# Kernel optimization log

Hardware: AMD Instinct MI355X
Metric: run time of the kernel (lower is better)

Reference implementation:

```python
import jax, jax.numpy as jnp
import numpy as np

B, S, D, H = 4, 2048, 1024, 16
DH = D // H


def setup_inputs() -> dict:
    key = jax.random.key(0)
    ks = jax.random.split(key, 10)
    init = lambda k, shape: jax.random.normal(k, shape, dtype=jnp.float32) * 0.02
    return {
        "x": jax.random.normal(ks[0], (B, S, D), dtype=jnp.float32),
        "attention_mask": jnp.ones((B, S), dtype=bool),
        "use_causal_mask": 1,
        "Wq": init(ks[1], (D, D)), "bq": jnp.zeros((D,), jnp.float32),
        "Wk": init(ks[2], (D, D)), "bk": jnp.zeros((D,), jnp.float32),
        "Wv": init(ks[3], (D, D)), "bv": jnp.zeros((D,), jnp.float32),
        "Wo": init(ks[4], (D, D)), "bo": jnp.zeros((D,), jnp.float32),
    }


def _split_heads(t):
    # (B, S, D) -> (B, H, S, DH)
    b, s, d = t.shape
    return t.reshape(b, s, H, DH).transpose(0, 2, 1, 3)


def reference(x, attention_mask, use_causal_mask, Wq, bq, Wk, bk, Wv, bv, Wo, bo):
    q = _split_heads(x @ Wq + bq)  # (B, H, S, DH)
    k = _split_heads(x @ Wk + bk)
    v = _split_heads(x @ Wv + bv)

    scale = 1.0 / jnp.sqrt(jnp.asarray(DH, dtype=x.dtype))
    scores = jnp.einsum("bhqd,bhkd->bhqk", q, k) * scale  # (B, H, S, S)

    blocked = jnp.finfo(scores.dtype).min
    if use_causal_mask:
        causal = jnp.tril(jnp.ones((S, S), dtype=bool))[None, None]
        scores = jnp.where(causal, scores, blocked)
    # attention_mask: (B, S) over keys
    scores = jnp.where(attention_mask[:, None, None, :], scores, blocked)

    weights = jax.nn.softmax(scores, axis=-1)
    attn = jnp.einsum("bhqk,bhkd->bhqd", weights, v)  # (B, H, S, DH)
    attn = attn.transpose(0, 2, 1, 3).reshape(B, S, D)  # combine heads
    return attn @ Wo + bo
```

## Files before the change

### kernel.cpp

```cpp
#include <hip/hip_runtime.h>
#include <hip/hip_bf16.h>
#include <cstdint>
#include <cstddef>


#define BB 4
#define SS 2048
#define DD 1024
#define HH 16
#define DHH 64

typedef float f32x4 __attribute__((ext_vector_type(4)));
typedef __bf16 bf16x8 __attribute__((ext_vector_type(8)));

#define QSCALE 0.1803368801111204f

__device__ __forceinline__ unsigned short f2bf(float f) {
  union { __hip_bfloat16 h; unsigned short u; } cv;
  cv.h = __float2bfloat16(f);
  return cv.u;
}

__device__ __forceinline__ float fexp2(float x) { return __builtin_amdgcn_exp2f(x); }

__device__ __forceinline__ void gload_lds16(const void* g, void* l) {
  __builtin_amdgcn_global_load_lds((const __attribute__((address_space(1))) void*)g,
                                   (__attribute__((address_space(3))) void*)l,
                                   16, 0, 0);
}

__device__ __forceinline__ void wait_vm4() { asm volatile("s_waitcnt vmcnt(4)" ::: "memory"); }
__device__ __forceinline__ void wait_vm8() { asm volatile("s_waitcnt vmcnt(8)" ::: "memory"); }
__device__ __forceinline__ void wait_vm0() { asm volatile("s_waitcnt vmcnt(0)" ::: "memory"); }
__device__ __forceinline__ void block_barrier() {
  asm volatile("" ::: "memory");
  __builtin_amdgcn_s_barrier();
  asm volatile("" ::: "memory");
}

__global__ void k_f32_to_bf16(const float* __restrict__ in,
                              unsigned short* __restrict__ out, int n8) {
  int i = blockIdx.x * blockDim.x + threadIdx.x;
  if (i >= n8) return;
  const float4* p = (const float4*)in + (size_t)i * 2;
  float4 a = p[0], b = p[1];
  union { unsigned short u[8]; uint4 v; } r;
  r.u[0] = f2bf(a.x); r.u[1] = f2bf(a.y); r.u[2] = f2bf(a.z); r.u[3] = f2bf(a.w);
  r.u[4] = f2bf(b.x); r.u[5] = f2bf(b.y); r.u[6] = f2bf(b.z); r.u[7] = f2bf(b.w);
  ((uint4*)out)[i] = r.v;
}

__global__ void k_transpose_w4(const float* __restrict__ Wq, const float* __restrict__ Wk,
                               const float* __restrict__ Wv, const float* __restrict__ Wo,
                               unsigned short* __restrict__ Wqkvt,
                               unsigned short* __restrict__ Wot) {
  __shared__ float t[64][65];
  const int z = blockIdx.z;
  const float* W = (z == 0) ? Wq : (z == 1) ? Wk : (z == 2) ? Wv : Wo;
  unsigned short* dst = (z < 3) ? (Wqkvt + (size_t)z * DD * DD) : Wot;
  int bx = blockIdx.x * 64;
  int by = blockIdx.y * 64;
  int c  = threadIdx.x & 63;
  int r0 = threadIdx.x >> 6;
#pragma unroll
  for (int r = r0; r < 64; r += 4)
    t[r][c] = W[(size_t)(by + r) * DD + bx + c];
  __syncthreads();
#pragma unroll
  for (int r = r0; r < 64; r += 4)
    dst[(size_t)(bx + r) * DD + by + c] = f2bf(t[c][r]);
}

template <int MODE, int GN>
__global__ __launch_bounds__(256) void k_gemm(const unsigned short* __restrict__ A,
                                              const unsigned short* __restrict__ Bt,
                                              const float* __restrict__ b0,
                                              const float* __restrict__ b1,
                                              const float* __restrict__ b2,
                                              void* __restrict__ out0,
                                              void* __restrict__ out1,
                                              void* __restrict__ out2) {
  constexpr int Kd = 1024;
  constexpr int NSTEP = Kd / 64;
  __shared__ unsigned short As[2][128 * 64];
  __shared__ unsigned short Bs[2][128 * 64];
  const int tid = threadIdx.x;
  const int wave = tid >> 6, lane = tid & 63;
  const int hw = blockIdx.x;
  const int xcd = hw & 7;
  const int j = hw >> 3;
  const int super = j >> 6;
  const int rem = j & 63;
  const int bm = (xcd * 8 + (rem >> 3)) * 128;
  const int bn = (super * 8 + (rem & 7)) * 128;
  const int wm = (wave >> 1) * 64, wn = (wave & 1) * 64;

  f32x4 acc[4][4] = {};

  const int srow = wave * 8 + (lane >> 3);
  const int csw = lane & 7;

  auto stage = [&](int buf, int k0) {
#pragma unroll
    for (int q = 0; q < 4; q++) {
      int r = q * 32 + srow;
      int clog = csw ^ (r & 7);
      gload_lds16(A + (size_t)(bm + r) * Kd + k0 + clog * 8, &As[buf][q * 2048 + wave * 512]);
      gload_lds16(Bt + (size_t)(bn + r) * Kd + k0 + clog * 8, &Bs[buf][q * 2048 + wave * 512]);
    }
  };

  stage(0, 0);
  for (int ks = 0; ks < NSTEP; ks++) {
    if (ks + 1 < NSTEP) {
      stage((ks + 1) & 1, (ks + 1) * 64);
      wait_vm8();
    } else {
      wait_vm0();
    }
    block_barrier();
    const unsigned short* Asb = As[ks & 1];
    const unsigned short* Bsb = Bs[ks & 1];
#pragma unroll
    for (int kk = 0; kk < 2; kk++) {
      bf16x8 af[4], bfr[4];
      int ch = (kk << 2) | (lane >> 4);
#pragma unroll
      for (int i = 0; i < 4; i++) {
        int row = wm + i * 16 + (lane & 15);
        af[i] = *(const bf16x8*)&Asb[row * 64 + ((ch ^ (row & 7)) << 3)];
      }
#pragma unroll
      for (int j2 = 0; j2 < 4; j2++) {
        int col = wn + j2 * 16 + (lane & 15);
        bfr[j2] = *(const bf16x8*)&Bsb[col * 64 + ((ch ^ (col & 7)) << 3)];
      }
#pragma unroll
      for (int i = 0; i < 4; i++)
#pragma unroll
        for (int j2 = 0; j2 < 4; j2++)
          acc[i][j2] = __builtin_amdgcn_mfma_f32_16x16x32_bf16(af[i], bfr[j2], acc[i][j2], 0, 0, 0);
    }
    block_barrier();
  }

  const int mat = bn >> 10;
  const float* bias = (MODE == 2) ? b0 : (mat == 0 ? b0 : (mat == 1 ? b1 : b2));
  const float scale = (MODE == 0 && mat == 0) ? QSCALE : 1.0f;
#pragma unroll
  for (int i = 0; i < 4; i++) {
#pragma unroll
    for (int j2 = 0; j2 < 4; j2++) {
      int col = bn + wn + j2 * 16 + (lane & 15);
      int c2 = col & 1023;
      float bv = bias[MODE == 2 ? col : c2];
      int row0 = bm + wm + i * 16 + ((lane >> 4) << 2);
      if (MODE == 0 && mat == 2) {
        int b = row0 >> 11, s0 = row0 & 2047, h = c2 >> 6, dh = c2 & 63;
        ushort4 pk;
        pk.x = f2bf(acc[i][j2][0] + bv);
        pk.y = f2bf(acc[i][j2][1] + bv);
        pk.z = f2bf(acc[i][j2][2] + bv);
        pk.w = f2bf(acc[i][j2][3] + bv);
        *(ushort4*)((unsigned short*)out2 + (((size_t)(b * HH + h) * DHH + dh) << 11) + s0) = pk;
      } else {
#pragma unroll
        for (int reg = 0; reg < 4; reg++) {
          int row = row0 + reg;
          float v = (acc[i][j2][reg] + bv) * scale;
          if (MODE == 0) {
            int b = row >> 11, s = row & 2047, h = c2 >> 6, dh = c2 & 63;
            unsigned short* dst = (unsigned short*)(mat == 0 ? out0 : out1);
            dst[(((size_t)(b * HH + h) * SS + s) << 6) + dh] = f2bf(v);
          } else {
            ((float*)out0)[(size_t)row * DD + col] = v;
          }
        }
      }
    }
  }
}

__global__ __launch_bounds__(256) void k_attn(const unsigned short* __restrict__ Q,
                                              const unsigned short* __restrict__ Kb,
                                              const unsigned short* __restrict__ Vt,
                                              unsigned short* __restrict__ O,
                                              const int* __restrict__ use_causal) {
  __shared__ unsigned short Ks[2][64 * 64];
  __shared__ unsigned short Vs[2][64 * 64];
  __shared__ unsigned short Ps[4 * 16 * 64];
  const int hw = blockIdx.x;
  const int bh = (hw & 7) | ((hw >> 7) << 3);
  const int pr = (hw >> 3) & 15;
  const int b = bh >> 4, h = bh & 15;
  const int tid = threadIdx.x, wave = tid >> 6, lane = tid & 63;
  const int lanelo = lane & 15, lanehi = lane >> 4;
  const bool causal = (use_causal[0] != 0);

  const unsigned short* Kg = Kb + (size_t)bh * SS * DHH;
  const unsigned short* Vg = Vt + (size_t)bh * DHH * SS;
  const int srow = wave * 8 + (lane >> 3);
  const int csw = lane & 7;
  const int qlocal = wave * 16 + lanelo;

  auto stage = [&](int buf, int kt) {
#pragma unroll
    for (int q = 0; q < 2; q++) {
      int r = q * 32 + srow;
      int clog = csw ^ (r & 7);
      gload_lds16(Kg + (size_t)(kt * 64 + r) * DHH + clog * 8, &Ks[buf][q * 2048 + wave * 512]);
      gload_lds16(Vg + (size_t)r * SS + kt * 64 + clog * 8, &Vs[buf][q * 2048 + wave * 512]);
    }
  };

  for (int pass = 0; pass < 2; pass++) {
    const int qt = pass ? (SS / 64 - 1 - pr) : pr;
    const unsigned short* Qg = Q + ((size_t)bh * SS + qt * 64) * DHH;

    bf16x8 qf0, qf1;
    {
      const unsigned short* qrow = Qg + (wave * 16 + lanelo) * DHH + (lanehi << 3);
      qf0 = *(const bf16x8*)qrow;
      qf1 = *(const bf16x8*)(qrow + 32);
    }

    float m = -1e30f, ls = 0.f;
    f32x4 o[4] = {};
    const int ntile = causal ? (qt + 1) : (SS / 64);

    stage(0, 0);
    for (int kt = 0; kt < ntile; kt++) {
      if (kt + 1 < ntile) {
        stage((kt + 1) & 1, kt + 1);
        wait_vm4();
      } else {
        wait_vm0();
      }
      block_barrier();
      const unsigned short* Ksb = Ks[kt & 1];
      const unsigned short* Vsb = Vs[kt & 1];

      f32x4 scT[4];
#pragma unroll
      for (int kb = 0; kb < 4; kb++) {
        int key = kb * 16 + lanelo;
        bf16x8 a0 = *(const bf16x8*)&Ksb[key * 64 + ((lanehi ^ (key & 7)) << 3)];
        bf16x8 a1 = *(const bf16x8*)&Ksb[key * 64 + (((lanehi + 4) ^ (key & 7)) << 3)];
        f32x4 t = {};
        t = __builtin_amdgcn_mfma_f32_16x16x32_bf16(a0, qf0, t, 0, 0, 0);
        t = __builtin_amdgcn_mfma_f32_16x16x32_bf16(a1, qf1, t, 0, 0, 0);
        scT[kb] = t;
      }

      const bool needmask = causal && (kt == qt);
      float mx = -3.0e38f;
#pragma unroll
      for (int kb = 0; kb < 4; kb++)
#pragma unroll
        for (int reg = 0; reg < 4; reg++) {
          float v = scT[kb][reg];
          if (needmask && (kb * 16 + 4 * lanehi + reg) > qlocal) v = -3.0e38f;
          scT[kb][reg] = v;
          mx = fmaxf(mx, v);
        }

      if (__any((int)(mx > m + 8.0f))) {
        float rmx = fmaxf(mx, __shfl_xor(mx, 16, 64));
        rmx = fmaxf(rmx, __shfl_xor(rmx, 32, 64));
        float mnew = fmaxf(m, rmx);
        float al = fexp2(m - mnew);
        m = mnew;
        ls *= al;
        float alr[4];
#pragma unroll
        for (int reg = 0; reg < 4; reg++)
          alr[reg] = __shfl(al, (lanehi << 2) + reg, 64);
#pragma unroll
        for (int dhb = 0; dhb < 4; dhb++) {
          f32x4 t = o[dhb];
          t[0] *= alr[0]; t[1] *= alr[1]; t[2] *= alr[2]; t[3] *= alr[3];
          o[dhb] = t;
        }
      }

      unsigned short* Pw = &Ps[wave * 1024];
#pragma unroll
      for (int kb = 0; kb < 4; kb++) {
        ushort4 pk;
        float p0 = fexp2(scT[kb][0] - m);
        float p1 = fexp2(scT[kb][1] - m);
        float p2 = fexp2(scT[kb][2] - m);
        float p3 = fexp2(scT[kb][3] - m);
        ls += (p0 + p1) + (p2 + p3);
        pk.x = f2bf(p0); pk.y = f2bf(p1); pk.z = f2bf(p2); pk.w = f2bf(p3);
        int chunk = (kb * 2 + (lanehi >> 1)) ^ (lanelo & 7);
        *(ushort4*)&Pw[lanelo * 64 + (chunk << 3) + ((lanehi & 1) << 2)] = pk;
      }

      int ar = lanelo;
      bf16x8 pa0 = *(const bf16x8*)&Pw[ar * 64 + ((lanehi ^ (ar & 7)) << 3)];
      bf16x8 pa1 = *(const bf16x8*)&Pw[ar * 64 + (((lanehi + 4) ^ (ar & 7)) << 3)];
#pragma unroll
      for (int dhb = 0; dhb < 4; dhb++) {
        int dh = dhb * 16 + lanelo;
        bf16x8 v0 = *(const bf16x8*)&Vsb[dh * 64 + ((lanehi ^ (dh & 7)) << 3)];
        bf16x8 v1 = *(const bf16x8*)&Vsb[dh * 64 + (((lanehi + 4) ^ (dh & 7)) << 3)];
        o[dhb] = __builtin_amdgcn_mfma_f32_16x16x32_bf16(pa0, v0, o[dhb], 0, 0, 0);
        o[dhb] = __builtin_amdgcn_mfma_f32_16x16x32_bf16(pa1, v1, o[dhb], 0, 0, 0);
      }
      block_barrier();
    }

    float t = ls + __shfl_xor(ls, 16, 64);
    t += __shfl_xor(t, 32, 64);
    float inv = 1.0f / t;
    float invr[4];
#pragma unroll
    for (int reg = 0; reg < 4; reg++)
      invr[reg] = __shfl(inv, (lanehi << 2) + reg, 64);
#pragma unroll
    for (int dhb = 0; dhb < 4; dhb++)
#pragma unroll
      for (int reg = 0; reg < 4; reg++) {
        int s = qt * 64 + wave * 16 + (lanehi << 2) + reg;
        int dh = dhb * 16 + lanelo;
        O[((size_t)(b * SS + s)) * DD + h * DHH + dh] = f2bf(o[dhb][reg] * invr[reg]);
      }
  }
}

extern "C" void kernel_launch(void* const* d_in, const int* in_sizes, int n_in,
                              void* d_out, int out_size, void* d_ws, size_t ws_size,
                              hipStream_t stream) {
  const float* x = (const float*)d_in[0];
  const int* use_causal = (const int*)d_in[2];
  const float* Wq = (const float*)d_in[3];
  const float* bq = (const float*)d_in[4];
  const float* Wk = (const float*)d_in[5];
  const float* bk = (const float*)d_in[6];
  const float* Wv = (const float*)d_in[7];
  const float* bv = (const float*)d_in[8];
  const float* Wo = (const float*)d_in[9];
  const float* bo = (const float*)d_in[10];

  char* ws = (char*)d_ws;
  unsigned short* xb    = (unsigned short*)(ws);
  unsigned short* Wqkvt = (unsigned short*)(ws + (16ull << 20));
  unsigned short* Wot   = (unsigned short*)(ws + (22ull << 20));
  unsigned short* Qb    = (unsigned short*)(ws + (24ull << 20));
  unsigned short* Kbuf  = (unsigned short*)(ws + (40ull << 20));
  unsigned short* Vtb   = (unsigned short*)(ws + (56ull << 20));
  unsigned short* Attn  = (unsigned short*)(ws + (72ull << 20));

  int n8 = BB * SS * DD / 8;
  k_f32_to_bf16<<<(n8 + 255) / 256, 256, 0, stream>>>(x, xb, n8);

  k_transpose_w4<<<dim3(16, 16, 4), 256, 0, stream>>>(Wq, Wk, Wv, Wo, Wqkvt, Wot);

  k_gemm<0, 24><<<dim3(64 * 24), 256, 0, stream>>>(xb, Wqkvt, bq, bk, bv, Qb, Kbuf, Vtb);

  k_attn<<<dim3(1024), 256, 0, stream>>>(Qb, Kbuf, Vtb, Attn, use_causal);

  k_gemm<2, 8><<<dim3(64 * 8), 256, 0, stream>>>(Attn, Wot, bo, nullptr, nullptr, d_out, nullptr, nullptr);
}
```

Before: 173.6 us.

## Use two waves per attention block, each computing 32 query rows

Measured after the change: 175.3 us. No clear change (+1.0%).

```diff
diff --git a/kernel.cpp b/kernel.cpp
--- a/kernel.cpp
+++ b/kernel.cpp
@@ -181,7 +181,7 @@
   }
 }
 
-__global__ __launch_bounds__(256) void k_attn(const unsigned short* __restrict__ Q,
+__global__ __launch_bounds__(128) void k_attn(const unsigned short* __restrict__ Q,
                                               const unsigned short* __restrict__ Kb,
                                               const unsigned short* __restrict__ Vt,
                                               unsigned short* __restrict__ O,
@@ -199,40 +199,40 @@
 
   const unsigned short* Kg = Kb + (size_t)bh * SS * DHH;
   const unsigned short* Vg = Vt + (size_t)bh * DHH * SS;
-  const int srow = wave * 8 + (lane >> 3);
+  const int srow8 = wave * 8 + (lane >> 3);
   const int csw = lane & 7;
-  const int qlocal = wave * 16 + lanelo;
 
   auto stage = [&](int buf, int kt) {
 #pragma unroll
-    for (int q = 0; q < 2; q++) {
-      int r = q * 32 + srow;
+    for (int q = 0; q < 4; q++) {
+      int r = q * 16 + srow8;
       int clog = csw ^ (r & 7);
-      gload_lds16(Kg + (size_t)(kt * 64 + r) * DHH + clog * 8, &Ks[buf][q * 2048 + wave * 512]);
-      gload_lds16(Vg + (size_t)r * SS + kt * 64 + clog * 8, &Vs[buf][q * 2048 + wave * 512]);
+      gload_lds16(Kg + (size_t)(kt * 64 + r) * DHH + clog * 8, &Ks[buf][q * 1024 + wave * 512]);
+      gload_lds16(Vg + (size_t)r * SS + kt * 64 + clog * 8, &Vs[buf][q * 1024 + wave * 512]);
     }
   };
 
   for (int pass = 0; pass < 2; pass++) {
-    const int qt = pass ? (SS / 64 - 1 - pr) : pr;
+    const int qt = pass ? (31 - pr) : pr;
     const unsigned short* Qg = Q + ((size_t)bh * SS + qt * 64) * DHH;
 
-    bf16x8 qf0, qf1;
-    {
-      const unsigned short* qrow = Qg + (wave * 16 + lanelo) * DHH + (lanehi << 3);
-      qf0 = *(const bf16x8*)qrow;
-      qf1 = *(const bf16x8*)(qrow + 32);
-    }
-
-    float m = -1e30f, ls = 0.f;
-    f32x4 o[4] = {};
-    const int ntile = causal ? (qt + 1) : (SS / 64);
+    bf16x8 qf[2][2];
+#pragma unroll
+    for (int qb = 0; qb < 2; qb++) {
+      const unsigned short* qrow = Qg + (wave * 32 + qb * 16 + lanelo) * DHH + (lanehi << 3);
+      qf[qb][0] = *(const bf16x8*)qrow;
+      qf[qb][1] = *(const bf16x8*)(qrow + 32);
+    }
+
+    float m[2] = {-1e30f, -1e30f}, ls[2] = {0.f, 0.f};
+    f32x4 o[2][4] = {};
+    const int ntile = causal ? (qt + 1) : 32;
 
     stage(0, 0);
     for (int kt = 0; kt < ntile; kt++) {
       if (kt + 1 < ntile) {
         stage((kt + 1) & 1, kt + 1);
-        wait_vm4();
+        wait_vm8();
       } else {
         wait_vm0();
       }
@@ -240,92 +240,122 @@
       const unsigned short* Ksb = Ks[kt & 1];
       const unsigned short* Vsb = Vs[kt & 1];
 
-      f32x4 scT[4];
+      f32x4 scT[2][4];
+      __builtin_amdgcn_s_setprio(1);
 #pragma unroll
       for (int kb = 0; kb < 4; kb++) {
         int key = kb * 16 + lanelo;
         bf16x8 a0 = *(const bf16x8*)&Ksb[key * 64 + ((lanehi ^ (key & 7)) << 3)];
         bf16x8 a1 = *(const bf16x8*)&Ksb[key * 64 + (((lanehi + 4) ^ (key & 7)) << 3)];
-        f32x4 t = {};
-        t = __builtin_amdgcn_mfma_f32_16x16x32_bf16(a0, qf0, t, 0, 0, 0);
-        t = __builtin_amdgcn_mfma_f32_16x16x32_bf16(a1, qf1, t, 0, 0, 0);
-        scT[kb] = t;
-      }
+        f32x4 t0 = {}, t1 = {};
+        t0 = __builtin_amdgcn_mfma_f32_16x16x32_bf16(a0, qf[0][0], t0, 0, 0, 0);
+        t0 = __builtin_amdgcn_mfma_f32_16x16x32_bf16(a1, qf[0][1], t0, 0, 0, 0);
+        t1 = __builtin_amdgcn_mfma_f32_16x16x32_bf16(a0, qf[1][0], t1, 0, 0, 0);
+        t1 = __builtin_amdgcn_mfma_f32_16x16x32_bf16(a1, qf[1][1], t1, 0, 0, 0);
+        scT[0][kb] = t0;
+        scT[1][kb] = t1;
+      }
+      __builtin_amdgcn_s_setprio(0);
 
       const bool needmask = causal && (kt == qt);
-      float mx = -3.0e38f;
-#pragma unroll
-      for (int kb = 0; kb < 4; kb++)
-#pragma unroll
-        for (int reg = 0; reg < 4; reg++) {
-          float v = scT[kb][reg];
-          if (needmask && (kb * 16 + 4 * lanehi + reg) > qlocal) v = -3.0e38f;
-          scT[kb][reg] = v;
-          mx = fmaxf(mx, v);
+      float mx[2];
+      bool need = false;
+#pragma unroll
+      for (int qb = 0; qb < 2; qb++) {
+        int qlocal = wave * 32 + qb * 16 + lanelo;
+        float x = -3.0e38f;
+#pragma unroll
+        for (int kb = 0; kb < 4; kb++)
+#pragma unroll
+          for (int reg = 0; reg < 4; reg++) {
+            float v = scT[qb][kb][reg];
+            if (needmask && (kb * 16 + 4 * lanehi + reg) > qlocal) v = -3.0e38f;
+            scT[qb][kb][reg] = v;
+            x = fmaxf(x, v);
+          }
+        mx[qb] = x;
+        need = need || (x > m[qb] + 8.0f);
+      }
+
+      if (__any((int)need)) {
+#pragma unroll
+        for (int qb = 0; qb < 2; qb++) {
+          float rmx = fmaxf(mx[qb], __shfl_xor(mx[qb], 16, 64));
+          rmx = fmaxf(rmx, __shfl_xor(rmx, 32, 64));
+          float mnew = fmaxf(m[qb], rmx);
+          float al = fexp2(m[qb] - mnew);
+          m[qb] = mnew;
+          ls[qb] *= al;
+          float alr[4];
+#pragma unroll
+          for (int reg = 0; reg < 4; reg++)
+            alr[reg] = __shfl(al, (lanehi << 2) + reg, 64);
+#pragma unroll
+          for (int dhb = 0; dhb < 4; dhb++) {
+            f32x4 t = o[qb][dhb];
+            t[0] *= alr[0]; t[1] *= alr[1]; t[2] *= alr[2]; t[3] *= alr[3];
+            o[qb][dhb] = t;
+          }
         }
-
-      if (__any((int)(mx > m + 8.0f))) {
-        float rmx = fmaxf(mx, __shfl_xor(mx, 16, 64));
-        rmx = fmaxf(rmx, __shfl_xor(rmx, 32, 64));
-        float mnew = fmaxf(m, rmx);
-        float al = fexp2(m - mnew);
-        m = mnew;
-        ls *= al;
-        float alr[4];
-#pragma unroll
-        for (int reg = 0; reg < 4; reg++)
-          alr[reg] = __shfl(al, (lanehi << 2) + reg, 64);
-#pragma unroll
-        for (int dhb = 0; dhb < 4; dhb++) {
-          f32x4 t = o[dhb];
-          t[0] *= alr[0]; t[1] *= alr[1]; t[2] *= alr[2]; t[3] *= alr[3];
-          o[dhb] = t;
+      }
+
+#pragma unroll
+      for (int qb = 0; qb < 2; qb++) {
+        unsigned short* Pw = &Ps[(wave * 2 + qb) * 1024];
+#pragma unroll
+        for (int kb = 0; kb < 4; kb++) {
+          float p0 = fexp2(scT[qb][kb][0] - m[qb]);
+          float p1 = fexp2(scT[qb][kb][1] - m[qb]);
+          float p2 = fexp2(scT[qb][kb][2] - m[qb]);
+          float p3 = fexp2(scT[qb][kb][3] - m[qb]);
+          ls[qb] += (p0 + p1) + (p2 + p3);
+          ushort4 pk;
+          pk.x = f2bf(p0); pk.y = f2bf(p1); pk.z = f2bf(p2); pk.w = f2bf(p3);
+          int chunk = (kb * 2 + (lanehi >> 1)) ^ (lanelo & 7);
+          *(ushort4*)&Pw[lanelo * 64 + (chunk << 3) + ((lanehi & 1) << 2)] = pk;
         }
       }
 
-      unsigned short* Pw = &Ps[wave * 1024];
-#pragma unroll
-      for (int kb = 0; kb < 4; kb++) {
-        ushort4 pk;
-        float p0 = fexp2(scT[kb][0] - m);
-        float p1 = fexp2(scT[kb][1] - m);
-        float p2 = fexp2(scT[kb][2] - m);
-        float p3 = fexp2(scT[kb][3] - m);
-        ls += (p0 + p1) + (p2 + p3);
-        pk.x = f2bf(p0); pk.y = f2bf(p1); pk.z = f2bf(p2); pk.w = f2bf(p3);
-        int chunk = (kb * 2 + (lanehi >> 1)) ^ (lanelo & 7);
-        *(ushort4*)&Pw[lanelo * 64 + (chunk << 3) + ((lanehi & 1) << 2)] = pk;
-      }
-
-      int ar = lanelo;
-      bf16x8 pa0 = *(const bf16x8*)&Pw[ar * 64 + ((lanehi ^ (ar & 7)) << 3)];
-      bf16x8 pa1 = *(const bf16x8*)&Pw[ar * 64 + (((lanehi + 4) ^ (ar & 7)) << 3)];
+      bf16x8 pa[2][2];
+#pragma unroll
+      for (int qb = 0; qb < 2; qb++) {
+        const unsigned short* Pw = &Ps[(wave * 2 + qb) * 1024];
+        pa[qb][0] = *(const bf16x8*)&Pw[lanelo * 64 + ((lanehi ^ (lanelo & 7)) << 3)];
+        pa[qb][1] = *(const bf16x8*)&Pw[lanelo * 64 + (((lanehi + 4) ^ (lanelo & 7)) << 3)];
+      }
+      __builtin_amdgcn_s_setprio(1);
 #pragma unroll
       for (int dhb = 0; dhb < 4; dhb++) {
         int dh = dhb * 16 + lanelo;
         bf16x8 v0 = *(const bf16x8*)&Vsb[dh * 64 + ((lanehi ^ (dh & 7)) << 3)];
         bf16x8 v1 = *(const bf16x8*)&Vsb[dh * 64 + (((lanehi + 4) ^ (dh & 7)) << 3)];
-        o[dhb] = __builtin_amdgcn_mfma_f32_16x16x32_bf16(pa0, v0, o[dhb], 0, 0, 0);
-        o[dhb] = __builtin_amdgcn_mfma_f32_16x16x32_bf16(pa1, v1, o[dhb], 0, 0, 0);
-      }
+        o[0][dhb] = __builtin_amdgcn_mfma_f32_16x16x32_bf16(pa[0][0], v0, o[0][dhb], 0, 0, 0);
+        o[0][dhb] = __builtin_amdgcn_mfma_f32_16x16x32_bf16(pa[0][1], v1, o[0][dhb], 0, 0, 0);
+        o[1][dhb] = __builtin_amdgcn_mfma_f32_16x16x32_bf16(pa[1][0], v0, o[1][dhb], 0, 0, 0);
+        o[1][dhb] = __builtin_amdgcn_mfma_f32_16x16x32_bf16(pa[1][1], v1, o[1][dhb], 0, 0, 0);
+      }
+      __builtin_amdgcn_s_setprio(0);
       block_barrier();
     }
 
-    float t = ls + __shfl_xor(ls, 16, 64);
-    t += __shfl_xor(t, 32, 64);
-    float inv = 1.0f / t;
-    float invr[4];
-#pragma unroll
-    for (int reg = 0; reg < 4; reg++)
-      invr[reg] = __shfl(inv, (lanehi << 2) + reg, 64);
-#pragma unroll
-    for (int dhb = 0; dhb < 4; dhb++)
-#pragma unroll
-      for (int reg = 0; reg < 4; reg++) {
-        int s = qt * 64 + wave * 16 + (lanehi << 2) + reg;
-        int dh = dhb * 16 + lanelo;
-        O[((size_t)(b * SS + s)) * DD + h * DHH + dh] = f2bf(o[dhb][reg] * invr[reg]);
-      }
+#pragma unroll
+    for (int qb = 0; qb < 2; qb++) {
+      float t = ls[qb] + __shfl_xor(ls[qb], 16, 64);
+      t += __shfl_xor(t, 32, 64);
+      float inv = 1.0f / t;
+      float invr[4];
+#pragma unroll
+      for (int reg = 0; reg < 4; reg++)
+        invr[reg] = __shfl(inv, (lanehi << 2) + reg, 64);
+#pragma unroll
+      for (int dhb = 0; dhb < 4; dhb++)
+#pragma unroll
+        for (int reg = 0; reg < 4; reg++) {
+          int s = qt * 64 + wave * 32 + qb * 16 + (lanehi << 2) + reg;
+          int dh = dhb * 16 + lanelo;
+          O[((size_t)(b * SS + s)) * DD + h * DHH + dh] = f2bf(o[qb][dhb][reg] * invr[reg]);
+        }
+    }
   }
 }
 
@@ -359,7 +389,7 @@
 
   k_gemm<0, 24><<<dim3(64 * 24), 256, 0, stream>>>(xb, Wqkvt, bq, bk, bv, Qb, Kbuf, Vtb);
 
-  k_attn<<<dim3(1024), 256, 0, stream>>>(Qb, Kbuf, Vtb, Attn, use_causal);
+  k_attn<<<dim3(1024), 128, 0, stream>>>(Qb, Kbuf, Vtb, Attn, use_causal);
 
   k_gemm<2, 8><<<dim3(64 * 8), 256, 0, stream>>>(Attn, Wot, bo, nullptr, nullptr, d_out, nullptr, nullptr);
 }
```

## Fuse paired causal query tiles into one pass sharing K/V tile loads

Applied to the files above, without the earlier changes.

Result: slower. 195.1 us (+12.4%).

```diff
diff --git a/kernel.cpp b/kernel.cpp
--- a/kernel.cpp
+++ b/kernel.cpp
@@ -203,6 +203,10 @@
   const int csw = lane & 7;
   const int qlocal = wave * 16 + lanelo;
 
+  const int qt0 = pr, qt1 = 31 - pr;
+  const int kA = causal ? qt0 : 31;
+  const int kend = causal ? qt1 : 31;
+
   auto stage = [&](int buf, int kt) {
 #pragma unroll
     for (int q = 0; q < 2; q++) {
@@ -213,105 +217,167 @@
     }
   };
 
-  for (int pass = 0; pass < 2; pass++) {
-    const int qt = pass ? (SS / 64 - 1 - pr) : pr;
-    const unsigned short* Qg = Q + ((size_t)bh * SS + qt * 64) * DHH;
-
-    bf16x8 qf0, qf1;
-    {
-      const unsigned short* qrow = Qg + (wave * 16 + lanelo) * DHH + (lanehi << 3);
-      qf0 = *(const bf16x8*)qrow;
-      qf1 = *(const bf16x8*)(qrow + 32);
-    }
-
-    float m = -1e30f, ls = 0.f;
-    f32x4 o[4] = {};
-    const int ntile = causal ? (qt + 1) : (SS / 64);
-
-    stage(0, 0);
-    for (int kt = 0; kt < ntile; kt++) {
-      if (kt + 1 < ntile) {
-        stage((kt + 1) & 1, kt + 1);
-        wait_vm4();
-      } else {
-        wait_vm0();
-      }
-      block_barrier();
-      const unsigned short* Ksb = Ks[kt & 1];
-      const unsigned short* Vsb = Vs[kt & 1];
-
-      f32x4 scT[4];
-#pragma unroll
-      for (int kb = 0; kb < 4; kb++) {
-        int key = kb * 16 + lanelo;
-        bf16x8 a0 = *(const bf16x8*)&Ksb[key * 64 + ((lanehi ^ (key & 7)) << 3)];
-        bf16x8 a1 = *(const bf16x8*)&Ksb[key * 64 + (((lanehi + 4) ^ (key & 7)) << 3)];
-        f32x4 t = {};
-        t = __builtin_amdgcn_mfma_f32_16x16x32_bf16(a0, qf0, t, 0, 0, 0);
-        t = __builtin_amdgcn_mfma_f32_16x16x32_bf16(a1, qf1, t, 0, 0, 0);
-        scT[kb] = t;
-      }
-
-      const bool needmask = causal && (kt == qt);
+  bf16x8 qfA0, qfA1, qfB0, qfB1;
+  {
+    const unsigned short* qa = Q + ((size_t)bh * SS + qt0 * 64 + wave * 16 + lanelo) * DHH + (lanehi << 3);
+    qfA0 = *(const bf16x8*)qa;
+    qfA1 = *(const bf16x8*)(qa + 32);
+    const unsigned short* qb = Q + ((size_t)bh * SS + qt1 * 64 + wave * 16 + lanelo) * DHH + (lanehi << 3);
+    qfB0 = *(const bf16x8*)qb;
+    qfB1 = *(const bf16x8*)(qb + 32);
+  }
+
+  float mA = -1e30f, lsA = 0.f, mB = -1e30f, lsB = 0.f;
+  f32x4 oA[4] = {}, oB[4] = {};
+
+  stage(0, 0);
+  for (int kt = 0; kt <= kend; kt++) {
+    if (kt < kend) {
+      stage((kt + 1) & 1, kt + 1);
+      wait_vm4();
+    } else {
+      wait_vm0();
+    }
+    block_barrier();
+    const unsigned short* Ksb = Ks[kt & 1];
+    const unsigned short* Vsb = Vs[kt & 1];
+    const bool doA = (kt <= kA);
+
+    f32x4 sA[4], sB[4];
+    __builtin_amdgcn_s_setprio(1);
+#pragma unroll
+    for (int kb = 0; kb < 4; kb++) {
+      int key = kb * 16 + lanelo;
+      bf16x8 a0 = *(const bf16x8*)&Ksb[key * 64 + ((lanehi ^ (key & 7)) << 3)];
+      bf16x8 a1 = *(const bf16x8*)&Ksb[key * 64 + (((lanehi + 4) ^ (key & 7)) << 3)];
+      f32x4 t = {};
+      t = __builtin_amdgcn_mfma_f32_16x16x32_bf16(a0, qfB0, t, 0, 0, 0);
+      t = __builtin_amdgcn_mfma_f32_16x16x32_bf16(a1, qfB1, t, 0, 0, 0);
+      sB[kb] = t;
+      if (doA) {
+        f32x4 u = {};
+        u = __builtin_amdgcn_mfma_f32_16x16x32_bf16(a0, qfA0, u, 0, 0, 0);
+        u = __builtin_amdgcn_mfma_f32_16x16x32_bf16(a1, qfA1, u, 0, 0, 0);
+        sA[kb] = u;
+      }
+    }
+    __builtin_amdgcn_s_setprio(0);
+
+    unsigned short* Pw = &Ps[wave * 1024];
+    bf16x8 paA0, paA1, paB0, paB1;
+
+    if (doA) {
+      const bool needmask = causal && (kt == qt0);
       float mx = -3.0e38f;
 #pragma unroll
       for (int kb = 0; kb < 4; kb++)
 #pragma unroll
         for (int reg = 0; reg < 4; reg++) {
-          float v = scT[kb][reg];
+          float v = sA[kb][reg];
           if (needmask && (kb * 16 + 4 * lanehi + reg) > qlocal) v = -3.0e38f;
-          scT[kb][reg] = v;
+          sA[kb][reg] = v;
           mx = fmaxf(mx, v);
         }
-
-      if (__any((int)(mx > m + 8.0f))) {
+      if (__any((int)(mx > mA + 8.0f))) {
         float rmx = fmaxf(mx, __shfl_xor(mx, 16, 64));
         rmx = fmaxf(rmx, __shfl_xor(rmx, 32, 64));
-        float mnew = fmaxf(m, rmx);
-        float al = fexp2(m - mnew);
-        m = mnew;
-        ls *= al;
+        float mnew = fmaxf(mA, rmx);
+        float al = fexp2(mA - mnew);
+        mA = mnew;
+        lsA *= al;
         float alr[4];
 #pragma unroll
         for (int reg = 0; reg < 4; reg++)
           alr[reg] = __shfl(al, (lanehi << 2) + reg, 64);
 #pragma unroll
         for (int dhb = 0; dhb < 4; dhb++) {
-          f32x4 t = o[dhb];
+          f32x4 t = oA[dhb];
           t[0] *= alr[0]; t[1] *= alr[1]; t[2] *= alr[2]; t[3] *= alr[3];
-          o[dhb] = t;
+          oA[dhb] = t;
         }
       }
-
-      unsigned short* Pw = &Ps[wave * 1024];
 #pragma unroll
       for (int kb = 0; kb < 4; kb++) {
+        float p0 = fexp2(sA[kb][0] - mA);
+        float p1 = fexp2(sA[kb][1] - mA);
+        float p2 = fexp2(sA[kb][2] - mA);
+        float p3 = fexp2(sA[kb][3] - mA);
+        lsA += (p0 + p1) + (p2 + p3);
         ushort4 pk;
-        float p0 = fexp2(scT[kb][0] - m);
-        float p1 = fexp2(scT[kb][1] - m);
-        float p2 = fexp2(scT[kb][2] - m);
-        float p3 = fexp2(scT[kb][3] - m);
-        ls += (p0 + p1) + (p2 + p3);
         pk.x = f2bf(p0); pk.y = f2bf(p1); pk.z = f2bf(p2); pk.w = f2bf(p3);
         int chunk = (kb * 2 + (lanehi >> 1)) ^ (lanelo & 7);
         *(ushort4*)&Pw[lanelo * 64 + (chunk << 3) + ((lanehi & 1) << 2)] = pk;
       }
-
-      int ar = lanelo;
-      bf16x8 pa0 = *(const bf16x8*)&Pw[ar * 64 + ((lanehi ^ (ar & 7)) << 3)];
-      bf16x8 pa1 = *(const bf16x8*)&Pw[ar * 64 + (((lanehi + 4) ^ (ar & 7)) << 3)];
-#pragma unroll
-      for (int dhb = 0; dhb < 4; dhb++) {
-        int dh = dhb * 16 + lanelo;
-        bf16x8 v0 = *(const bf16x8*)&Vsb[dh * 64 + ((lanehi ^ (dh & 7)) << 3)];
-        bf16x8 v1 = *(const bf16x8*)&Vsb[dh * 64 + (((lanehi + 4) ^ (dh & 7)) << 3)];
-        o[dhb] = __builtin_amdgcn_mfma_f32_16x16x32_bf16(pa0, v0, o[dhb], 0, 0, 0);
-        o[dhb] = __builtin_amdgcn_mfma_f32_16x16x32_bf16(pa1, v1, o[dhb], 0, 0, 0);
-      }
-      block_barrier();
-    }
-
-    float t = ls + __shfl_xor(ls, 16, 64);
+      paA0 = *(const bf16x8*)&Pw[lanelo * 64 + ((lanehi ^ (lanelo & 7)) << 3)];
+      paA1 = *(const bf16x8*)&Pw[lanelo * 64 + (((lanehi + 4) ^ (lanelo & 7)) << 3)];
+    }
+
+    {
+      const bool needmask = causal && (kt == qt1);
+      float mx = -3.0e38f;
+#pragma unroll
+      for (int kb = 0; kb < 4; kb++)
+#pragma unroll
+        for (int reg = 0; reg < 4; reg++) {
+          float v = sB[kb][reg];
+          if (needmask && (kb * 16 + 4 * lanehi + reg) > qlocal) v = -3.0e38f;
+          sB[kb][reg] = v;
+          mx = fmaxf(mx, v);
+        }
+      if (__any((int)(mx > mB + 8.0f))) {
+        float rmx = fmaxf(mx, __shfl_xor(mx, 16, 64));
+        rmx = fmaxf(rmx, __shfl_xor(rmx, 32, 64));
+        float mnew = fmaxf(mB, rmx);
+        float al = fexp2(mB - mnew);
+        mB = mnew;
+        lsB *= al;
+        float alr[4];
+#pragma unroll
+        for (int reg = 0; reg < 4; reg++)
+          alr[reg] = __shfl(al, (lanehi << 2) + reg, 64);
+#pragma unroll
+        for (int dhb = 0; dhb < 4; dhb++) {
+          f32x4 t = oB[dhb];
+          t[0] *= alr[0]; t[1] *= alr[1]; t[2] *= alr[2]; t[3] *= alr[3];
+          oB[dhb] = t;
+        }
+      }
+      asm volatile("" ::: "memory");
+#pragma unroll
+      for (int kb = 0; kb < 4; kb++) {
+        float p0 = fexp2(sB[kb][0] - mB);
+        float p1 = fexp2(sB[kb][1] - mB);
+        float p2 = fexp2(sB[kb][2] - mB);
+        float p3 = fexp2(sB[kb][3] - mB);
+        lsB += (p0 + p1) + (p2 + p3);
+        ushort4 pk;
+        pk.x = f2bf(p0); pk.y = f2bf(p1); pk.z = f2bf(p2); pk.w = f2bf(p3);
+        int chunk = (kb * 2 + (lanehi >> 1)) ^ (lanelo & 7);
+        *(ushort4*)&Pw[lanelo * 64 + (chunk << 3) + ((lanehi & 1) << 2)] = pk;
+      }
+      paB0 = *(const bf16x8*)&Pw[lanelo * 64 + ((lanehi ^ (lanelo & 7)) << 3)];
+      paB1 = *(const bf16x8*)&Pw[lanelo * 64 + (((lanehi + 4) ^ (lanelo & 7)) << 3)];
+    }
+
+    __builtin_amdgcn_s_setprio(1);
+#pragma unroll
+    for (int dhb = 0; dhb < 4; dhb++) {
+      int dh = dhb * 16 + lanelo;
+      bf16x8 v0 = *(const bf16x8*)&Vsb[dh * 64 + ((lanehi ^ (dh & 7)) << 3)];
+      bf16x8 v1 = *(const bf16x8*)&Vsb[dh * 64 + (((lanehi + 4) ^ (dh & 7)) << 3)];
+      oB[dhb] = __builtin_amdgcn_mfma_f32_16x16x32_bf16(paB0, v0, oB[dhb], 0, 0, 0);
+      oB[dhb] = __builtin_amdgcn_mfma_f32_16x16x32_bf16(paB1, v1, oB[dhb], 0, 0, 0);
+      if (doA) {
+        oA[dhb] = __builtin_amdgcn_mfma_f32_16x16x32_bf16(paA0, v0, oA[dhb], 0, 0, 0);
+        oA[dhb] = __builtin_amdgcn_mfma_f32_16x16x32_bf16(paA1, v1, oA[dhb], 0, 0, 0);
+      }
+    }
+    __builtin_amdgcn_s_setprio(0);
+    block_barrier();
+  }
+
+  {
+    float t = lsA + __shfl_xor(lsA, 16, 64);
     t += __shfl_xor(t, 32, 64);
     float inv = 1.0f / t;
     float invr[4];
@@ -322,9 +388,26 @@
     for (int dhb = 0; dhb < 4; dhb++)
 #pragma unroll
       for (int reg = 0; reg < 4; reg++) {
-        int s = qt * 64 + wave * 16 + (lanehi << 2) + reg;
+        int s = qt0 * 64 + wave * 16 + (lanehi << 2) + reg;
         int dh = dhb * 16 + lanelo;
-        O[((size_t)(b * SS + s)) * DD + h * DHH + dh] = f2bf(o[dhb][reg] * invr[reg]);
+        O[((size_t)(b * SS + s)) * DD + h * DHH + dh] = f2bf(oA[dhb][reg] * invr[reg]);
+      }
+  }
+  {
+    float t = lsB + __shfl_xor(lsB, 16, 64);
+    t += __shfl_xor(t, 32, 64);
+    float inv = 1.0f / t;
+    float invr[4];
+#pragma unroll
+    for (int reg = 0; reg < 4; reg++)
+      invr[reg] = __shfl(inv, (lanehi << 2) + reg, 64);
+#pragma unroll
+    for (int dhb = 0; dhb < 4; dhb++)
+#pragma unroll
+      for (int reg = 0; reg < 4; reg++) {
+        int s = qt1 * 64 + wave * 16 + (lanehi << 2) + reg;
+        int dh = dhb * 16 + lanelo;
+        O[((size_t)(b * SS + s)) * DD + h * DHH + dh] = f2bf(oB[dhb][reg] * invr[reg]);
       }
   }
 }
```

## Compute softmax row sums via MFMA with ones vector and add setprio hints

Applied to the files above, without the earlier changes.

Result: no change. 172.6 us (-0.6%).

```diff
diff --git a/kernel.cpp b/kernel.cpp
--- a/kernel.cpp
+++ b/kernel.cpp
@@ -203,6 +203,10 @@
   const int csw = lane & 7;
   const int qlocal = wave * 16 + lanelo;
 
+  bf16x8 vones;
+#pragma unroll
+  for (int i = 0; i < 8; i++) vones[i] = (__bf16)1.0f;
+
   auto stage = [&](int buf, int kt) {
 #pragma unroll
     for (int q = 0; q < 2; q++) {
@@ -224,8 +228,9 @@
       qf1 = *(const bf16x8*)(qrow + 32);
     }
 
-    float m = -1e30f, ls = 0.f;
+    float m = -1e30f;
     f32x4 o[4] = {};
+    f32x4 o_ls = {};
     const int ntile = causal ? (qt + 1) : (SS / 64);
 
     stage(0, 0);
@@ -241,6 +246,7 @@
       const unsigned short* Vsb = Vs[kt & 1];
 
       f32x4 scT[4];
+      __builtin_amdgcn_s_setprio(1);
 #pragma unroll
       for (int kb = 0; kb < 4; kb++) {
         int key = kb * 16 + lanelo;
@@ -251,18 +257,28 @@
         t = __builtin_amdgcn_mfma_f32_16x16x32_bf16(a1, qf1, t, 0, 0, 0);
         scT[kb] = t;
       }
-
-      const bool needmask = causal && (kt == qt);
-      float mx = -3.0e38f;
-#pragma unroll
-      for (int kb = 0; kb < 4; kb++)
-#pragma unroll
-        for (int reg = 0; reg < 4; reg++) {
-          float v = scT[kb][reg];
-          if (needmask && (kb * 16 + 4 * lanehi + reg) > qlocal) v = -3.0e38f;
-          scT[kb][reg] = v;
-          mx = fmaxf(mx, v);
-        }
+      __builtin_amdgcn_s_setprio(0);
+
+      float mx;
+      if (causal && (kt == qt)) {
+        mx = -3.0e38f;
+#pragma unroll
+        for (int kb = 0; kb < 4; kb++)
+#pragma unroll
+          for (int reg = 0; reg < 4; reg++) {
+            float v = scT[kb][reg];
+            if ((kb * 16 + 4 * lanehi + reg) > qlocal) v = -3.0e38f;
+            scT[kb][reg] = v;
+            mx = fmaxf(mx, v);
+          }
+      } else {
+        float t0 = fmaxf(fmaxf(scT[0][0], scT[0][1]), scT[0][2]);
+        float t1 = fmaxf(fmaxf(scT[0][3], scT[1][0]), scT[1][1]);
+        float t2 = fmaxf(fmaxf(scT[1][2], scT[1][3]), scT[2][0]);
+        float t3 = fmaxf(fmaxf(scT[2][1], scT[2][2]), scT[2][3]);
+        float t4 = fmaxf(fmaxf(scT[3][0], scT[3][1]), scT[3][2]);
+        mx = fmaxf(fmaxf(fmaxf(t0, t1), t2), fmaxf(fmaxf(t3, t4), scT[3][3]));
+      }
 
       if (__any((int)(mx > m + 8.0f))) {
         float rmx = fmaxf(mx, __shfl_xor(mx, 16, 64));
@@ -270,7 +286,6 @@
         float mnew = fmaxf(m, rmx);
         float al = fexp2(m - mnew);
         m = mnew;
-        ls *= al;
         float alr[4];
 #pragma unroll
         for (int reg = 0; reg < 4; reg++)
@@ -281,18 +296,17 @@
           t[0] *= alr[0]; t[1] *= alr[1]; t[2] *= alr[2]; t[3] *= alr[3];
           o[dhb] = t;
         }
+        o_ls[0] *= alr[0]; o_ls[1] *= alr[1]; o_ls[2] *= alr[2]; o_ls[3] *= alr[3];
       }
 
       unsigned short* Pw = &Ps[wave * 1024];
 #pragma unroll
       for (int kb = 0; kb < 4; kb++) {
         ushort4 pk;
-        float p0 = fexp2(scT[kb][0] - m);
-        float p1 = fexp2(scT[kb][1] - m);
-        float p2 = fexp2(scT[kb][2] - m);
-        float p3 = fexp2(scT[kb][3] - m);
-        ls += (p0 + p1) + (p2 + p3);
-        pk.x = f2bf(p0); pk.y = f2bf(p1); pk.z = f2bf(p2); pk.w = f2bf(p3);
+        pk.x = f2bf(fexp2(scT[kb][0] - m));
+        pk.y = f2bf(fexp2(scT[kb][1] - m));
+        pk.z = f2bf(fexp2(scT[kb][2] - m));
+        pk.w = f2bf(fexp2(scT[kb][3] - m));
         int chunk = (kb * 2 + (lanehi >> 1)) ^ (lanelo & 7);
         *(ushort4*)&Pw[lanelo * 64 + (chunk << 3) + ((lanehi & 1) << 2)] = pk;
       }
@@ -300,6 +314,9 @@
       int ar = lanelo;
       bf16x8 pa0 = *(const bf16x8*)&Pw[ar * 64 + ((lanehi ^ (ar & 7)) << 3)];
       bf16x8 pa1 = *(const bf16x8*)&Pw[ar * 64 + (((lanehi + 4) ^ (ar & 7)) << 3)];
+      __builtin_amdgcn_s_setprio(1);
+      o_ls = __builtin_amdgcn_mfma_f32_16x16x32_bf16(pa0, vones, o_ls, 0, 0, 0);
+      o_ls = __builtin_amdgcn_mfma_f32_16x16x32_bf16(pa1, vones, o_ls, 0, 0, 0);
 #pragma unroll
       for (int dhb = 0; dhb < 4; dhb++) {
         int dh = dhb * 16 + lanelo;
@@ -308,16 +325,13 @@
         o[dhb] = __builtin_amdgcn_mfma_f32_16x16x32_bf16(pa0, v0, o[dhb], 0, 0, 0);
         o[dhb] = __builtin_amdgcn_mfma_f32_16x16x32_bf16(pa1, v1, o[dhb], 0, 0, 0);
       }
+      __builtin_amdgcn_s_setprio(0);
       block_barrier();
     }
 
-    float t = ls + __shfl_xor(ls, 16, 64);
-    t += __shfl_xor(t, 32, 64);
-    float inv = 1.0f / t;
     float invr[4];
 #pragma unroll
-    for (int reg = 0; reg < 4; reg++)
-      invr[reg] = __shfl(inv, (lanehi << 2) + reg, 64);
+    for (int reg = 0; reg < 4; reg++) invr[reg] = 1.0f / o_ls[reg];
 #pragma unroll
     for (int dhb = 0; dhb < 4; dhb++)
 #pragma unroll
```
